# Optimization experiments

Measured on AMD Instinct MI355X. Metric: run time of the kernel, lower is better.

Reference implementation:

```python
import jax, jax.numpy as jnp
import numpy as np

LN_EPS = 1e-6  # flax LayerNorm default


def setup_inputs() -> dict:
    B, S, D, H, HD = 4, 2048, 1024, 16, 64
    key = jax.random.key(0)
    ks = jax.random.split(key, 3)
    x = jax.random.normal(ks[0], (B, S, D), dtype=jnp.float32)
    mask = jnp.tril(jnp.ones((S, S), dtype=bool))[None, None]  # causal [1,1,S,S]
    ln_scale = jnp.ones((D,), jnp.float32)
    ln_bias = jnp.zeros((D,), jnp.float32)
    w_qkv = jax.random.normal(ks[1], (D, H, 3 * HD), jnp.float32) * (1.0 / np.sqrt(D))
    b_qkv = jnp.zeros((H, 3 * HD), jnp.float32)
    w_out = jax.random.normal(ks[2], (D, D), jnp.float32) * (1.0 / np.sqrt(D))
    b_out = jnp.zeros((D,), jnp.float32)
    return {"x": x, "mask": mask, "ln_scale": ln_scale, "ln_bias": ln_bias,
            "w_qkv": w_qkv, "b_qkv": b_qkv, "w_out": w_out, "b_out": b_out}


def _layernorm(x, scale, bias):
    mu = jnp.mean(x, axis=-1, keepdims=True)
    var = jnp.var(x, axis=-1, keepdims=True)
    return (x - mu) * jax.lax.rsqrt(var + LN_EPS) * scale + bias


def reference(x, mask, ln_scale, ln_bias, w_qkv, b_qkv, w_out, b_out):
    B, S, D = x.shape
    xn = _layernorm(x, ln_scale, ln_bias)                      # [B,S,D]
    qkv = jnp.einsum('bsd,dhf->bshf', xn, w_qkv) + b_qkv        # [B,S,H,3*hd]
    q, k, v = jnp.split(qkv, 3, axis=-1)                        # each [B,S,H,hd]
    scale = q.shape[-1] ** (-0.5)
    q = q * scale
    q = q.transpose(0, 2, 1, 3)                                 # [B,H,S,hd]
    k = k.transpose(0, 2, 1, 3)
    v = v.transpose(0, 2, 1, 3)
    attn = q @ k.swapaxes(-2, -1)                               # [B,H,S,S]
    attn = jnp.where(mask, attn, jnp.finfo(jnp.float32).min)
    attn = jax.nn.softmax(attn, axis=-1)
    y = attn @ v                                                # [B,H,S,hd]
    y = y.transpose(0, 2, 1, 3).reshape(B, S, D)
    y = y @ w_out + b_out                                       # [B,S,D]
    return y
```

## Files before the change

kernel.cpp:

```cpp
#include <hip/hip_runtime.h>

typedef unsigned short u16;
typedef unsigned int u32;
typedef __bf16 bf16x8 __attribute__((ext_vector_type(8)));
typedef float f32x4 __attribute__((ext_vector_type(4)));
typedef u16 u16x8 __attribute__((ext_vector_type(8)));
typedef u16 u16x4 __attribute__((ext_vector_type(4)));

#define GLOBAL_AS __attribute__((address_space(1)))
#define LDS_AS __attribute__((address_space(3)))

#define LOG2E 1.4426950408889634f
#define SMAX_C 24.0f
#define SMAX_C2 34.62468097703102f

__device__ __forceinline__ void async16(const u16* g, u16* l) {
  __builtin_amdgcn_global_load_lds((const GLOBAL_AS void*)g, (LDS_AS void*)l, 16, 0, 0);
}

__device__ __forceinline__ float bf2f(u16 u) {
  union { unsigned int i; float f; } v; v.i = ((unsigned int)u) << 16; return v.f;
}
__device__ __forceinline__ u16 f2bf(float f) {
  __bf16 h = (__bf16)f;
  return __builtin_bit_cast(u16, h);
}

__device__ __forceinline__ int swz(int r, int c) {
  return r * 64 + (c ^ ((r & 7) << 3));
}

__global__ __launch_bounds__(256) void transpose_k(const float* __restrict__ in,
                                                   u16* __restrict__ out,
                                                   int R, int C) {
  __shared__ u16 tile[32][33];
  const int c0 = blockIdx.x * 32, r0 = blockIdx.y * 32;
  const int tx = threadIdx.x & 31, ty = threadIdx.x >> 5;
  #pragma unroll
  for (int i = 0; i < 32; i += 8)
    tile[ty + i][tx] = f2bf(in[(size_t)(r0 + ty + i) * C + c0 + tx]);
  __syncthreads();
  #pragma unroll
  for (int i = 0; i < 32; i += 8)
    out[(size_t)(c0 + ty + i) * R + r0 + tx] = tile[tx][ty + i];
}

__global__ __launch_bounds__(256) void ln_k(const float* __restrict__ x,
                                            const float* __restrict__ gamma,
                                            const float* __restrict__ beta,
                                            u16* __restrict__ xn) {
  const int rowid = blockIdx.x;
  const int t = threadIdx.x, wid = t >> 6, lane = t & 63;
  const float* xr = x + (size_t)rowid * 1024;
  float4 v = *(const float4*)&xr[t * 4];
  float s = v.x + v.y + v.z + v.w;
  float ss = v.x * v.x + v.y * v.y + v.z * v.z + v.w * v.w;
  #pragma unroll
  for (int off = 32; off >= 1; off >>= 1) {
    s += __shfl_xor(s, off, 64);
    ss += __shfl_xor(ss, off, 64);
  }
  __shared__ float red[8];
  if (lane == 0) { red[wid] = s; red[4 + wid] = ss; }
  __syncthreads();
  s = red[0] + red[1] + red[2] + red[3];
  ss = red[4] + red[5] + red[6] + red[7];
  const float mu = s * (1.0f / 1024.0f);
  const float var = ss * (1.0f / 1024.0f) - mu * mu;
  const float rstd = rsqrtf(var + 1e-6f);
  float4 gv = *(const float4*)&gamma[t * 4];
  float4 bv = *(const float4*)&beta[t * 4];
  ushort4 o;
  o.x = f2bf((v.x - mu) * rstd * gv.x + bv.x);
  o.y = f2bf((v.y - mu) * rstd * gv.y + bv.y);
  o.z = f2bf((v.z - mu) * rstd * gv.z + bv.z);
  o.w = f2bf((v.w - mu) * rstd * gv.w + bv.w);
  *(ushort4*)&xn[(size_t)rowid * 1024 + t * 4] = o;
}

template <typename OutT>
__global__ __launch_bounds__(256) void gemm_bt(const u16* __restrict__ A,
                                               const u16* __restrict__ Bt,
                                               const float* __restrict__ bias,
                                               OutT* __restrict__ C,
                                               int M, int N, int K) {
  __shared__ __align__(16) u16 As[3][128 * 32];
  __shared__ __align__(16) u16 Bs[3][128 * 32];
  const int tid = threadIdx.x, wid = tid >> 6, lane = tid & 63;
  const int row = lane & 15, q4 = lane >> 4;
  const int m0 = blockIdx.y * 128, n0 = blockIdx.x * 128;
  const int wm = (wid >> 1) * 64, wn = (wid & 1) * 64;
  f32x4 acc[4][4] = {};
  const int sr = wid * 16 + (lane >> 2);
  const int sk = (lane & 3) * 8;
  const u16* gA0 = A + (size_t)(m0 + sr) * K + sk;
  const u16* gA1 = A + (size_t)(m0 + 64 + sr) * K + sk;
  const u16* gB0 = Bt + (size_t)(n0 + sr) * K + sk;
  const u16* gB1 = Bt + (size_t)(n0 + 64 + sr) * K + sk;
  const int lw = wid * 512;
  const int NT = K >> 5;

  async16(gA0, &As[0][lw]);
  async16(gA1, &As[0][2048 + lw]);
  async16(gB0, &Bs[0][lw]);
  async16(gB1, &Bs[0][2048 + lw]);
  async16(gA0 + 32, &As[1][lw]);
  async16(gA1 + 32, &As[1][2048 + lw]);
  async16(gB0 + 32, &Bs[1][lw]);
  async16(gB1 + 32, &Bs[1][2048 + lw]);

  int bc = 0, bs = 2;
  for (int kt = 0; kt < NT; ++kt) {
    asm volatile("s_waitcnt vmcnt(4)" ::: "memory");
    __builtin_amdgcn_s_barrier();
    __builtin_amdgcn_sched_barrier(0);
    if (kt + 2 < NT) {
      const int k0 = (kt + 2) << 5;
      async16(gA0 + k0, &As[bs][lw]);
      async16(gA1 + k0, &As[bs][2048 + lw]);
      async16(gB0 + k0, &Bs[bs][lw]);
      async16(gB1 + k0, &Bs[bs][2048 + lw]);
    }
    __builtin_amdgcn_sched_barrier(0);
    bf16x8 af[4], bfv[4];
    #pragma unroll
    for (int mt = 0; mt < 4; ++mt)
      af[mt] = *(const bf16x8*)&As[bc][(wm + mt * 16 + row) * 32 + q4 * 8];
    #pragma unroll
    for (int nt = 0; nt < 4; ++nt)
      bfv[nt] = *(const bf16x8*)&Bs[bc][(wn + nt * 16 + row) * 32 + q4 * 8];
    #pragma unroll
    for (int mt = 0; mt < 4; ++mt)
      #pragma unroll
      for (int nt = 0; nt < 4; ++nt)
        acc[mt][nt] = __builtin_amdgcn_mfma_f32_16x16x32_bf16(
            af[mt], bfv[nt], acc[mt][nt], 0, 0, 0);
    bs = bc;
    bc = (bc + 1 == 3) ? 0 : bc + 1;
  }
  #pragma unroll
  for (int nt = 0; nt < 4; ++nt) {
    const int gn = n0 + wn + nt * 16 + row;
    const float bv = bias[gn];
    #pragma unroll
    for (int mt = 0; mt < 4; ++mt) {
      const int gm = m0 + wm + mt * 16 + q4 * 4;
      #pragma unroll
      for (int r = 0; r < 4; ++r) {
        const float val = acc[mt][nt][r] + bv;
        if constexpr (sizeof(OutT) == 2)
          C[(size_t)(gm + r) * N + gn] = (OutT)f2bf(val);
        else
          C[(size_t)(gm + r) * N + gn] = (OutT)val;
      }
    }
  }
}

__global__ __launch_bounds__(256, 3) void attn_k(const u16* __restrict__ qkv,
                                                 u16* __restrict__ y) {
  __shared__ __align__(16) u16 Ks[2][64 * 64];
  __shared__ __align__(16) u16 Vs[2][64 * 64];
  __shared__ __align__(16) u16 Ps[4][2][16 * 64];
  const int tid = threadIdx.x, wid = tid >> 6, lane = tid & 63;
  const int row = lane & 15, q4 = lane >> 4;
  const int id = blockIdx.x;
  const int qb = 15 - (id >> 6);
  const int h = (id & 63) >> 2, b = id & 3;
  const size_t seq0 = (size_t)b * 2048;
  const u16* base = qkv + seq0 * 3072 + h * 192;
  const int kk = tid >> 2, ko = tid & 3;
  const int kp = tid & 31, dg = tid >> 5;

  bf16x8 ones;
  #pragma unroll
  for (int j = 0; j < 8; ++j) ones[j] = (__bf16)1.0f;

  const int rgmin = qb * 128 + wid * 32;
  const int rgmax = rgmin + 31;
  bf16x8 qf[2][2];
  #pragma unroll
  for (int g = 0; g < 2; ++g) {
    const u16* qp = base + (size_t)(rgmin + g * 16 + row) * 3072;
    qf[g][0] = *(const bf16x8*)(qp + q4 * 8);
    qf[g][1] = *(const bf16x8*)(qp + 32 + q4 * 8);
    #pragma unroll
    for (int j = 0; j < 8; ++j) {
      qf[g][0][j] = (__bf16)((float)qf[g][0][j] * 0.125f);
      qf[g][1][j] = (__bf16)((float)qf[g][1][j] * 0.125f);
    }
  }
  f32x4 l4[2] = {};
  f32x4 o[2][4] = {};
  const int ktiles = 2 * qb + 2;

  const u16* kg = base + (size_t)kk * 3072 + 64 + ko * 8;
  const u16* vg = base + (size_t)(2 * kp) * 3072 + 128 + dg * 8;
  u16x8 kr0 = *(const u16x8*)kg;
  u16x8 kr1 = *(const u16x8*)(kg + 32);
  u16x8 va = *(const u16x8*)vg;
  u16x8 vb = *(const u16x8*)(vg + 3072);
  *(u16x8*)&Ks[0][swz(kk, ko * 8)] = kr0;
  *(u16x8*)&Ks[0][swz(kk, ko * 8 + 32)] = kr1;
  #pragma unroll
  for (int j = 0; j < 8; ++j)
    *(u32*)&Vs[0][swz(dg * 8 + j, 2 * kp)] = (u32)va[j] | ((u32)vb[j] << 16);
  if (ktiles > 1) {
    kr0 = *(const u16x8*)(kg + (size_t)64 * 3072);
    kr1 = *(const u16x8*)(kg + (size_t)64 * 3072 + 32);
    va = *(const u16x8*)(vg + (size_t)64 * 3072);
    vb = *(const u16x8*)(vg + (size_t)65 * 3072);
  }
  __syncthreads();

  for (int kt = 0; kt < ktiles; ++kt) {
    const int kbase = kt * 64;
    const int cur = kt & 1;
    if (kt + 1 < ktiles) {
      *(u16x8*)&Ks[cur ^ 1][swz(kk, ko * 8)] = kr0;
      *(u16x8*)&Ks[cur ^ 1][swz(kk, ko * 8 + 32)] = kr1;
      #pragma unroll
      for (int j = 0; j < 8; ++j)
        *(u32*)&Vs[cur ^ 1][swz(dg * 8 + j, 2 * kp)] =
            (u32)va[j] | ((u32)vb[j] << 16);
      if (kt + 2 < ktiles) {
        const size_t nb = (size_t)(kbase + 128) * 3072;
        kr0 = *(const u16x8*)(kg + nb);
        kr1 = *(const u16x8*)(kg + nb + 32);
        va = *(const u16x8*)(vg + nb);
        vb = *(const u16x8*)(vg + nb + 3072);
      }
    }

    if (kbase <= rgmax) {
      #pragma unroll
      for (int nt = 0; nt < 4; ++nt) {
        bf16x8 kf0 = *(const bf16x8*)&Ks[cur][swz(nt * 16 + row, q4 * 8)];
        bf16x8 kf1 = *(const bf16x8*)&Ks[cur][swz(nt * 16 + row, 32 + q4 * 8)];
        #pragma unroll
        for (int g = 0; g < 2; ++g) {
          f32x4 z = {0.f, 0.f, 0.f, 0.f};
          z = __builtin_amdgcn_mfma_f32_16x16x32_bf16(qf[g][0], kf0, z, 0, 0, 0);
          z = __builtin_amdgcn_mfma_f32_16x16x32_bf16(qf[g][1], kf1, z, 0, 0, 0);
          const int rb = rgmin + g * 16;
          const bool maskneed = (kbase + 63 > rb);
          u16* pw = Ps[wid][g];
          #pragma unroll
          for (int r = 0; r < 4; ++r) {
            float v = z[r];
            if (maskneed) {
              const int rg = rb + q4 * 4 + r;
              if (kbase + nt * 16 + row > rg) v = -1e30f;
            }
            const float p = __builtin_amdgcn_exp2f(
                fmaf(fminf(v, SMAX_C), LOG2E, -SMAX_C2));
            pw[swz(q4 * 4 + r, nt * 16 + row)] = f2bf(p);
          }
        }
      }

      bf16x8 pf[2][2];
      #pragma unroll
      for (int g = 0; g < 2; ++g) {
        pf[g][0] = *(const bf16x8*)&Ps[wid][g][swz(row, q4 * 8)];
        pf[g][1] = *(const bf16x8*)&Ps[wid][g][swz(row, 32 + q4 * 8)];
        l4[g] = __builtin_amdgcn_mfma_f32_16x16x32_bf16(pf[g][0], ones, l4[g], 0, 0, 0);
        l4[g] = __builtin_amdgcn_mfma_f32_16x16x32_bf16(pf[g][1], ones, l4[g], 0, 0, 0);
      }

      #pragma unroll
      for (int t = 0; t < 4; ++t) {
        bf16x8 vf0 = *(const bf16x8*)&Vs[cur][swz(t * 16 + row, q4 * 8)];
        bf16x8 vf1 = *(const bf16x8*)&Vs[cur][swz(t * 16 + row, 32 + q4 * 8)];
        #pragma unroll
        for (int g = 0; g < 2; ++g) {
          o[g][t] = __builtin_amdgcn_mfma_f32_16x16x32_bf16(pf[g][0], vf0, o[g][t], 0, 0, 0);
          o[g][t] = __builtin_amdgcn_mfma_f32_16x16x32_bf16(pf[g][1], vf1, o[g][t], 0, 0, 0);
        }
      }
    }
    __syncthreads();
  }

  #pragma unroll
  for (int g = 0; g < 2; ++g) {
    const int srow = rgmin + g * 16 + q4 * 4;
    float inv[4];
    #pragma unroll
    for (int r = 0; r < 4; ++r) inv[r] = 1.0f / l4[g][r];
    #pragma unroll
    for (int t = 0; t < 4; ++t)
      #pragma unroll
      for (int r = 0; r < 4; ++r)
        y[(seq0 + srow + r) * 1024 + h * 64 + t * 16 + row] =
            f2bf(o[g][t][r] * inv[r]);
  }
}

extern "C" void kernel_launch(void* const* d_in, const int* in_sizes, int n_in,
                              void* d_out, int out_size, void* d_ws, size_t ws_size,
                              hipStream_t stream) {
  const float* x     = (const float*)d_in[0];
  const float* ln_s  = (const float*)d_in[2];
  const float* ln_b  = (const float*)d_in[3];
  const float* w_qkv = (const float*)d_in[4];
  const float* b_qkv = (const float*)d_in[5];
  const float* w_out = (const float*)d_in[6];
  const float* b_out = (const float*)d_in[7];
  float* out = (float*)d_out;

  u16* qkv   = (u16*)d_ws;
  u16* xn    = qkv + (size_t)8192 * 3072;
  u16* wTq   = xn + (size_t)8192 * 1024;
  u16* wTo   = wTq + (size_t)3072 * 1024;
  u16* yattn = xn;

  transpose_k<<<dim3(96, 32), 256, 0, stream>>>(w_qkv, wTq, 1024, 3072);
  transpose_k<<<dim3(32, 32), 256, 0, stream>>>(w_out, wTo, 1024, 1024);
  ln_k<<<8192, 256, 0, stream>>>(x, ln_s, ln_b, xn);
  gemm_bt<u16><<<dim3(24, 64), 256, 0, stream>>>(xn, wTq, b_qkv, qkv, 8192, 3072, 1024);
  attn_k<<<1024, 256, 0, stream>>>(qkv, yattn);
  gemm_bt<float><<<dim3(8, 64), 256, 0, stream>>>(yattn, wTo, b_out, out, 8192, 1024, 1024);
}
```

Baseline: 274.6 us.

## Fuse prep kernels, shrink attention P buffer, raise occupancy, simplify masked exp

Merges the two weight transposes and the LayerNorm into one prep kernel launch, which removes launch overhead. In the attention kernel, the P scratch buffer is halved by processing the two row groups sequentially with a sched_barrier between them. Launch bounds rise to 4 blocks per CU. The masked exponent now folds the mask into an additive bias and drops the fminf clamp, which removes the guard against overflow in the fixed-offset softmax when scores exceed the old cap.

```diff
diff --git a/kernel.cpp b/kernel.cpp
--- a/kernel.cpp
+++ b/kernel.cpp
@@ -11,7 +11,6 @@
 #define LDS_AS __attribute__((address_space(3)))
 
 #define LOG2E 1.4426950408889634f
-#define SMAX_C 24.0f
 #define SMAX_C2 34.62468097703102f
 
 __device__ __forceinline__ void async16(const u16* g, u16* l) {
@@ -30,11 +29,50 @@
   return r * 64 + (c ^ ((r & 7) << 3));
 }
 
-__global__ __launch_bounds__(256) void transpose_k(const float* __restrict__ in,
-                                                   u16* __restrict__ out,
-                                                   int R, int C) {
+__global__ __launch_bounds__(256) void prep_k(const float* __restrict__ x,
+                                              const float* __restrict__ gamma,
+                                              const float* __restrict__ beta,
+                                              u16* __restrict__ xn,
+                                              const float* __restrict__ wq,
+                                              u16* __restrict__ wTq,
+                                              const float* __restrict__ wo,
+                                              u16* __restrict__ wTo) {
   __shared__ u16 tile[32][33];
-  const int c0 = blockIdx.x * 32, r0 = blockIdx.y * 32;
+  __shared__ float red[8];
+  int id = blockIdx.x;
+  if (id < 8192) {
+    const int t = threadIdx.x, wid = t >> 6, lane = t & 63;
+    const float* xr = x + (size_t)id * 1024;
+    float4 v = *(const float4*)&xr[t * 4];
+    float s = v.x + v.y + v.z + v.w;
+    float ss = v.x * v.x + v.y * v.y + v.z * v.z + v.w * v.w;
+    #pragma unroll
+    for (int off = 32; off >= 1; off >>= 1) {
+      s += __shfl_xor(s, off, 64);
+      ss += __shfl_xor(ss, off, 64);
+    }
+    if (lane == 0) { red[wid] = s; red[4 + wid] = ss; }
+    __syncthreads();
+    s = red[0] + red[1] + red[2] + red[3];
+    ss = red[4] + red[5] + red[6] + red[7];
+    const float mu = s * (1.0f / 1024.0f);
+    const float var = ss * (1.0f / 1024.0f) - mu * mu;
+    const float rstd = rsqrtf(var + 1e-6f);
+    float4 gv = *(const float4*)&gamma[t * 4];
+    float4 bv = *(const float4*)&beta[t * 4];
+    ushort4 o;
+    o.x = f2bf((v.x - mu) * rstd * gv.x + bv.x);
+    o.y = f2bf((v.y - mu) * rstd * gv.y + bv.y);
+    o.z = f2bf((v.z - mu) * rstd * gv.z + bv.z);
+    o.w = f2bf((v.w - mu) * rstd * gv.w + bv.w);
+    *(ushort4*)&xn[(size_t)id * 1024 + t * 4] = o;
+    return;
+  }
+  id -= 8192;
+  const float* in; u16* out; int R, C, bx, by;
+  if (id < 3072) { in = wq; out = wTq; R = 1024; C = 3072; bx = id % 96; by = id / 96; }
+  else { id -= 3072; in = wo; out = wTo; R = 1024; C = 1024; bx = id & 31; by = id >> 5; }
+  const int c0 = bx * 32, r0 = by * 32;
   const int tx = threadIdx.x & 31, ty = threadIdx.x >> 5;
   #pragma unroll
   for (int i = 0; i < 32; i += 8)
@@ -43,39 +81,6 @@
   #pragma unroll
   for (int i = 0; i < 32; i += 8)
     out[(size_t)(c0 + ty + i) * R + r0 + tx] = tile[tx][ty + i];
-}
-
-__global__ __launch_bounds__(256) void ln_k(const float* __restrict__ x,
-                                            const float* __restrict__ gamma,
-                                            const float* __restrict__ beta,
-                                            u16* __restrict__ xn) {
-  const int rowid = blockIdx.x;
-  const int t = threadIdx.x, wid = t >> 6, lane = t & 63;
-  const float* xr = x + (size_t)rowid * 1024;
-  float4 v = *(const float4*)&xr[t * 4];
-  float s = v.x + v.y + v.z + v.w;
-  float ss = v.x * v.x + v.y * v.y + v.z * v.z + v.w * v.w;
-  #pragma unroll
-  for (int off = 32; off >= 1; off >>= 1) {
-    s += __shfl_xor(s, off, 64);
-    ss += __shfl_xor(ss, off, 64);
-  }
-  __shared__ float red[8];
-  if (lane == 0) { red[wid] = s; red[4 + wid] = ss; }
-  __syncthreads();
-  s = red[0] + red[1] + red[2] + red[3];
-  ss = red[4] + red[5] + red[6] + red[7];
-  const float mu = s * (1.0f / 1024.0f);
-  const float var = ss * (1.0f / 1024.0f) - mu * mu;
-  const float rstd = rsqrtf(var + 1e-6f);
-  float4 gv = *(const float4*)&gamma[t * 4];
-  float4 bv = *(const float4*)&beta[t * 4];
-  ushort4 o;
-  o.x = f2bf((v.x - mu) * rstd * gv.x + bv.x);
-  o.y = f2bf((v.y - mu) * rstd * gv.y + bv.y);
-  o.z = f2bf((v.z - mu) * rstd * gv.z + bv.z);
-  o.w = f2bf((v.w - mu) * rstd * gv.w + bv.w);
-  *(ushort4*)&xn[(size_t)rowid * 1024 + t * 4] = o;
 }
 
 template <typename OutT>
@@ -157,11 +162,11 @@
   }
 }
 
-__global__ __launch_bounds__(256, 3) void attn_k(const u16* __restrict__ qkv,
+__global__ __launch_bounds__(256, 4) void attn_k(const u16* __restrict__ qkv,
                                                  u16* __restrict__ y) {
   __shared__ __align__(16) u16 Ks[2][64 * 64];
   __shared__ __align__(16) u16 Vs[2][64 * 64];
-  __shared__ __align__(16) u16 Ps[4][2][16 * 64];
+  __shared__ __align__(16) u16 Ps[4][16 * 64];
   const int tid = threadIdx.x, wid = tid >> 6, lane = tid & 63;
   const int row = lane & 15, q4 = lane >> 4;
   const int id = blockIdx.x;
@@ -233,39 +238,33 @@
     }
 
     if (kbase <= rgmax) {
-      #pragma unroll
-      for (int nt = 0; nt < 4; ++nt) {
-        bf16x8 kf0 = *(const bf16x8*)&Ks[cur][swz(nt * 16 + row, q4 * 8)];
-        bf16x8 kf1 = *(const bf16x8*)&Ks[cur][swz(nt * 16 + row, 32 + q4 * 8)];
+      bf16x8 pf[2][2];
+      u16* pw = Ps[wid];
+      #pragma unroll
+      for (int g = 0; g < 2; ++g) {
+        const int rb = rgmin + g * 16;
+        const bool mn = (kbase + 63 > rb);
+        const int dbase = kbase + row - rb - q4 * 4;
         #pragma unroll
-        for (int g = 0; g < 2; ++g) {
+        for (int nt = 0; nt < 4; ++nt) {
+          bf16x8 kf0 = *(const bf16x8*)&Ks[cur][swz(nt * 16 + row, q4 * 8)];
+          bf16x8 kf1 = *(const bf16x8*)&Ks[cur][swz(nt * 16 + row, 32 + q4 * 8)];
           f32x4 z = {0.f, 0.f, 0.f, 0.f};
           z = __builtin_amdgcn_mfma_f32_16x16x32_bf16(qf[g][0], kf0, z, 0, 0, 0);
           z = __builtin_amdgcn_mfma_f32_16x16x32_bf16(qf[g][1], kf1, z, 0, 0, 0);
-          const int rb = rgmin + g * 16;
-          const bool maskneed = (kbase + 63 > rb);
-          u16* pw = Ps[wid][g];
+          const int d = dbase + nt * 16;
           #pragma unroll
           for (int r = 0; r < 4; ++r) {
-            float v = z[r];
-            if (maskneed) {
-              const int rg = rb + q4 * 4 + r;
-              if (kbase + nt * 16 + row > rg) v = -1e30f;
-            }
-            const float p = __builtin_amdgcn_exp2f(
-                fmaf(fminf(v, SMAX_C), LOG2E, -SMAX_C2));
+            const float bias = (mn && d > r) ? -1e30f : -SMAX_C2;
+            const float p = __builtin_amdgcn_exp2f(fmaf(z[r], LOG2E, bias));
             pw[swz(q4 * 4 + r, nt * 16 + row)] = f2bf(p);
           }
         }
-      }
-
-      bf16x8 pf[2][2];
-      #pragma unroll
-      for (int g = 0; g < 2; ++g) {
-        pf[g][0] = *(const bf16x8*)&Ps[wid][g][swz(row, q4 * 8)];
-        pf[g][1] = *(const bf16x8*)&Ps[wid][g][swz(row, 32 + q4 * 8)];
+        pf[g][0] = *(const bf16x8*)&pw[swz(row, q4 * 8)];
+        pf[g][1] = *(const bf16x8*)&pw[swz(row, 32 + q4 * 8)];
         l4[g] = __builtin_amdgcn_mfma_f32_16x16x32_bf16(pf[g][0], ones, l4[g], 0, 0, 0);
         l4[g] = __builtin_amdgcn_mfma_f32_16x16x32_bf16(pf[g][1], ones, l4[g], 0, 0, 0);
+        __builtin_amdgcn_sched_barrier(0);
       }
 
       #pragma unroll
@@ -315,9 +314,7 @@
   u16* wTo   = wTq + (size_t)3072 * 1024;
   u16* yattn = xn;
 
-  transpose_k<<<dim3(96, 32), 256, 0, stream>>>(w_qkv, wTq, 1024, 3072);
-  transpose_k<<<dim3(32, 32), 256, 0, stream>>>(w_out, wTo, 1024, 1024);
-  ln_k<<<8192, 256, 0, stream>>>(x, ln_s, ln_b, xn);
+  prep_k<<<12288, 256, 0, stream>>>(x, ln_s, ln_b, xn, w_qkv, wTq, w_out, wTo);
   gemm_bt<u16><<<dim3(24, 64), 256, 0, stream>>>(xn, wTq, b_qkv, qkv, 8192, 3072, 1024);
   attn_k<<<1024, 256, 0, stream>>>(qkv, yattn);
   gemm_bt<float><<<dim3(8, 64), 256, 0, stream>>>(yattn, wTo, b_out, out, 8192, 1024, 1024);
```

Result: slower. 322.7 us (+17.5%).
